# Kernel tuning notes

Hardware: AMD Instinct MI355X
Metric: run time of the kernel (lower is better)

## Reference

```python
import jax, jax.numpy as jnp
import numpy as np

N, E, D, H = 50000, 800000, 128, 128


def setup_inputs() -> dict:
    key = jax.random.key(0)
    ks = jax.random.split(key, 8)
    x = jax.random.normal(ks[0], (N, D), dtype=jnp.float32)
    src = jax.random.randint(ks[1], (E,), 0, N, dtype=jnp.int64)
    dst = jax.random.randint(ks[2], (E,), 0, N, dtype=jnp.int64)
    s_in = 1.0 / np.sqrt(D)
    s_h = 1.0 / np.sqrt(H)
    return {
        "x": x,
        "src": src,
        "dst": dst,
        "W_self1": jax.random.normal(ks[3], (D, H), dtype=jnp.float32) * s_in,
        "W_neigh1": jax.random.normal(ks[4], (D, H), dtype=jnp.float32) * s_in,
        "b1": jnp.zeros((H,), dtype=jnp.float32),
        "W_self2": jax.random.normal(ks[5], (H, H), dtype=jnp.float32) * s_h,
        "W_neigh2": jax.random.normal(ks[6], (H, H), dtype=jnp.float32) * s_h,
        "b2": jnp.zeros((H,), dtype=jnp.float32),
    }


def _sage_conv(h, src, dst, n_nodes, W_self, W_neigh, b):
    # mean aggregation over in-neighbors: gather src feats, segment-sum by dst
    msg = jax.ops.segment_sum(h[src], dst, num_segments=n_nodes)  # [N, d]
    deg = jax.ops.segment_sum(jnp.ones((src.shape[0], 1), h.dtype), dst,
                              num_segments=n_nodes)               # [N, 1]
    h_neigh = msg / jnp.maximum(deg, 1.0)  # zero-degree nodes -> 0 (DGL clamps)
    return h @ W_self + h_neigh @ W_neigh + b


def reference(x, src, dst, W_self1, W_neigh1, b1, W_self2, W_neigh2, b2):
    n = x.shape[0]
    h = jax.nn.relu(_sage_conv(x, src, dst, n, W_self1, W_neigh1, b1))
    return _sage_conv(h, src, dst, n, W_self2, W_neigh2, b2)
```

## Files before the change

### kernel.cpp

```cpp
#include <hip/hip_runtime.h>

#define DH 128
#define SLOTS 64

typedef __bf16 bf16x8 __attribute__((ext_vector_type(8)));
typedef float f32x4 __attribute__((ext_vector_type(4)));
typedef float f32x2 __attribute__((ext_vector_type(2)));

__device__ __forceinline__ ushort f2b(float f) {
  union { float f; unsigned u; } c; c.f = f;
  unsigned u = c.u;
  unsigned r = (u + 0x7fffu + ((u >> 16) & 1u)) >> 16;
  return (ushort)r;
}
__device__ __forceinline__ unsigned char f2f8(float v) {
  return (unsigned char)(__builtin_amdgcn_cvt_pk_fp8_f32(v, v, 0, false) & 0xff);
}

__global__ void k_prep(int4* __restrict__ degz, int nZero, int nz4,
                       const float* __restrict__ x, ushort* __restrict__ xb,
                       uint2* __restrict__ xf8, long n8, int nConv,
                       const float* __restrict__ Ws1, const float* __restrict__ Wn1,
                       const float* __restrict__ Ws2, const float* __restrict__ Wn2,
                       ushort* __restrict__ Wp1, ushort* __restrict__ Wp2) {
  int bid = blockIdx.x;
  if (bid < nZero) {
    int i = bid * 256 + threadIdx.x;
    if (i < nz4) degz[i] = int4{0, 0, 0, 0};
  } else if (bid < nZero + nConv) {
    long i = (long)(bid - nZero) * 256 + threadIdx.x;
    if (i >= n8) return;
    const float4* p = (const float4*)x + i * 2;
    float4 a = p[0], b = p[1];
    uint4 o;
    o.x = (unsigned)f2b(a.x) | ((unsigned)f2b(a.y) << 16);
    o.y = (unsigned)f2b(a.z) | ((unsigned)f2b(a.w) << 16);
    o.z = (unsigned)f2b(b.x) | ((unsigned)f2b(b.y) << 16);
    o.w = (unsigned)f2b(b.z) | ((unsigned)f2b(b.w) << 16);
    ((uint4*)xb)[i] = o;
    int w0 = __builtin_amdgcn_cvt_pk_fp8_f32(a.x, a.y, 0, false);
    w0 = __builtin_amdgcn_cvt_pk_fp8_f32(a.z, a.w, w0, true);
    int w1 = __builtin_amdgcn_cvt_pk_fp8_f32(b.x, b.y, 0, false);
    w1 = __builtin_amdgcn_cvt_pk_fp8_f32(b.z, b.w, w1, true);
    xf8[i] = uint2{(unsigned)w0, (unsigned)w1};
  } else {
    int idx = (bid - nZero - nConv) * 256 + threadIdx.x;
    if (idx >= 2 * 8 * 8 * 64 * 8) return;
    int layer = idx >> 15;
    int t = idx & 32767;
    int j = t & 7;
    int lane = (t >> 3) & 63;
    int cb = (t >> 9) & 7;
    int s = (t >> 12) & 7;
    int col = cb * 16 + (lane & 15);
    int k = s * 32 + ((lane >> 4) * 8) + j;
    const float* Wself = layer ? Ws2 : Ws1;
    const float* Wneigh = layer ? Wn2 : Wn1;
    float v = (k < 128) ? Wself[k * 128 + col] : Wneigh[(k - 128) * 128 + col];
    (layer ? Wp2 : Wp1)[t] = f2b(v);
  }
}

__global__ void k_fill8p(const int* __restrict__ src, const int* __restrict__ dst,
                         int* __restrict__ deg, int* __restrict__ colsrc,
                         int E, int nper, int chunkSz) {
  int part = blockIdx.x & 7;
  int chunk = blockIdx.x >> 3;
  int lo = part * nper, hi = lo + nper;
  int base = chunk * chunkSz;
  int end = min(base + chunkSz, E);
  for (int i = base + threadIdx.x; i < end; i += 256) {
    int d = dst[i];
    int s = src[i];
    if (d >= lo && d < hi) {
      int r = atomicAdd(&deg[d], 1);
      if (r < SLOTS) colsrc[(size_t)d * SLOTS + r] = s;
    }
  }
}

__device__ __forceinline__ void acc8f8(float* a, uint2 v) {
  f32x2 p0 = __builtin_amdgcn_cvt_pk_f32_fp8(v.x, false);
  f32x2 p1 = __builtin_amdgcn_cvt_pk_f32_fp8(v.x, true);
  f32x2 p2 = __builtin_amdgcn_cvt_pk_f32_fp8(v.y, false);
  f32x2 p3 = __builtin_amdgcn_cvt_pk_f32_fp8(v.y, true);
  a[0] += p0.x; a[1] += p0.y; a[2] += p1.x; a[3] += p1.y;
  a[4] += p2.x; a[5] += p2.y; a[6] += p3.x; a[7] += p3.y;
}

template <int RELU, int OUTF32, int WRITEF8>
__global__ __launch_bounds__(1024, 8) void k_aggemm(
    const ushort* __restrict__ feat, const uint2* __restrict__ feat8,
    const int* __restrict__ deg, const int* __restrict__ colsrc,
    const ushort* __restrict__ Wp, const float* __restrict__ bias,
    void* __restrict__ outp, unsigned char* __restrict__ outf8, int M) {
  __shared__ ushort hn[64][136];
  int tid = threadIdx.x;

  {
    int g = tid >> 4, l = tid & 15;
    int node = blockIdx.x * 64 + g;
    float a[8] = {0.f, 0.f, 0.f, 0.f, 0.f, 0.f, 0.f, 0.f};
    float sc = 0.f;
    if (node < M) {
      int dd = min(deg[node], SLOTS);
      const int* cs = colsrc + (size_t)node * SLOTS;
      int e = 0;
      for (; e + 8 <= dd; e += 8) {
        int s0 = cs[e], s1 = cs[e + 1], s2 = cs[e + 2], s3 = cs[e + 3];
        int s4 = cs[e + 4], s5 = cs[e + 5], s6 = cs[e + 6], s7 = cs[e + 7];
        uint2 v0 = feat8[(size_t)s0 * 16 + l];
        uint2 v1 = feat8[(size_t)s1 * 16 + l];
        uint2 v2 = feat8[(size_t)s2 * 16 + l];
        uint2 v3 = feat8[(size_t)s3 * 16 + l];
        uint2 v4 = feat8[(size_t)s4 * 16 + l];
        uint2 v5 = feat8[(size_t)s5 * 16 + l];
        uint2 v6 = feat8[(size_t)s6 * 16 + l];
        uint2 v7 = feat8[(size_t)s7 * 16 + l];
        acc8f8(a, v0); acc8f8(a, v1); acc8f8(a, v2); acc8f8(a, v3);
        acc8f8(a, v4); acc8f8(a, v5); acc8f8(a, v6); acc8f8(a, v7);
      }
      for (; e + 4 <= dd; e += 4) {
        int s0 = cs[e], s1 = cs[e + 1], s2 = cs[e + 2], s3 = cs[e + 3];
        uint2 v0 = feat8[(size_t)s0 * 16 + l];
        uint2 v1 = feat8[(size_t)s1 * 16 + l];
        uint2 v2 = feat8[(size_t)s2 * 16 + l];
        uint2 v3 = feat8[(size_t)s3 * 16 + l];
        acc8f8(a, v0); acc8f8(a, v1); acc8f8(a, v2); acc8f8(a, v3);
      }
      for (; e < dd; ++e) acc8f8(a, feat8[(size_t)cs[e] * 16 + l]);
      sc = 1.0f / fmaxf((float)dd, 1.0f);
    }
    uint4 o;
    o.x = (unsigned)f2b(a[0] * sc) | ((unsigned)f2b(a[1] * sc) << 16);
    o.y = (unsigned)f2b(a[2] * sc) | ((unsigned)f2b(a[3] * sc) << 16);
    o.z = (unsigned)f2b(a[4] * sc) | ((unsigned)f2b(a[5] * sc) << 16);
    o.w = (unsigned)f2b(a[6] * sc) | ((unsigned)f2b(a[7] * sc) << 16);
    *(uint4*)&hn[g][l * 8] = o;
  }
  __syncthreads();

  int wave = tid >> 6, lane = tid & 63;
  int rg = wave >> 2;
  int cb0 = (wave & 3) * 2;
  int rowA = blockIdx.x * 64 + rg * 16 + (lane & 15);
  int kq = lane >> 4;
  bool valid = rowA < M;
  size_t abase = (size_t)rowA * DH + kq * 8;
  int lrow = rg * 16 + (lane & 15);
  f32x4 acc0 = {}, acc1 = {};
#pragma unroll
  for (int hf = 0; hf < 2; ++hf) {
#pragma unroll
    for (int ks = 0; ks < 4; ++ks) {
      bf16x8 a = {};
      if (hf == 0) {
        if (valid) a = __builtin_bit_cast(bf16x8, *(const uint4*)(feat + abase + ks * 32));
      } else {
        a = __builtin_bit_cast(bf16x8, *(const uint4*)&hn[lrow][ks * 32 + kq * 8]);
      }
      int sg = hf * 4 + ks;
      const ushort* wp = Wp + sg * 4096 + lane * 8;
      bf16x8 b0 = __builtin_bit_cast(bf16x8, *(const uint4*)(wp + cb0 * 512));
      bf16x8 b1 = __builtin_bit_cast(bf16x8, *(const uint4*)(wp + (cb0 + 1) * 512));
      acc0 = __builtin_amdgcn_mfma_f32_16x16x32_bf16(a, b0, acc0, 0, 0, 0);
      acc1 = __builtin_amdgcn_mfma_f32_16x16x32_bf16(a, b1, acc1, 0, 0, 0);
    }
  }
  int col = lane & 15;
  int row0 = blockIdx.x * 64 + rg * 16 + (lane >> 4) * 4;
#pragma unroll
  for (int t = 0; t < 2; ++t) {
    int cb = cb0 + t;
    float bv = bias[cb * 16 + col];
    f32x4 acc = t ? acc1 : acc0;
#pragma unroll
    for (int j = 0; j < 4; ++j) {
      int rr = row0 + j;
      if (rr < M) {
        float v = acc[j] + bv;
        if (RELU) v = fmaxf(v, 0.f);
        if (OUTF32)
          ((float*)outp)[(size_t)rr * DH + cb * 16 + col] = v;
        else
          ((ushort*)outp)[(size_t)rr * DH + cb * 16 + col] = f2b(v);
        if (WRITEF8)
          outf8[(size_t)rr * DH + cb * 16 + col] = f2f8(v);
      }
    }
  }
}

extern "C" void kernel_launch(void* const* d_in, const int* in_sizes, int n_in,
                              void* d_out, int out_size, void* d_ws, size_t ws_size,
                              hipStream_t stream) {
  const float* x = (const float*)d_in[0];
  const int* src = (const int*)d_in[1];
  const int* dst = (const int*)d_in[2];
  const float* Wself1 = (const float*)d_in[3];
  const float* Wneigh1 = (const float*)d_in[4];
  const float* b1 = (const float*)d_in[5];
  const float* Wself2 = (const float*)d_in[6];
  const float* Wneigh2 = (const float*)d_in[7];
  const float* b2 = (const float*)d_in[8];
  int N = in_sizes[0] / DH;
  int E = in_sizes[1];

  char* w = (char*)d_ws;
  auto alloc = [&](size_t bytes) {
    char* p = w;
    w += (bytes + 255) & ~(size_t)255;
    return p;
  };
  ushort* xb = (ushort*)alloc((size_t)N * DH * 2);
  ushort* hb = (ushort*)alloc((size_t)N * DH * 2);
  unsigned char* xf8 = (unsigned char*)alloc((size_t)N * DH);
  unsigned char* hf8 = (unsigned char*)alloc((size_t)N * DH);
  ushort* Wp1 = (ushort*)alloc(32768 * 2);
  ushort* Wp2 = (ushort*)alloc(32768 * 2);
  int* deg = (int*)alloc((size_t)N * 4);
  int* colsrc = (int*)alloc((size_t)N * SLOTS * 4);

  int nz4 = (N + 3) / 4;
  int nZero = (nz4 + 255) / 256;
  long n8 = (long)N * DH / 8;
  int nConv = (int)((n8 + 255) / 256);
  int nPack = (2 * 8 * 8 * 64 * 8 + 255) / 256;
  k_prep<<<nZero + nConv + nPack, 256, 0, stream>>>(
      (int4*)deg, nZero, nz4, x, xb, (uint2*)xf8, n8, nConv,
      Wself1, Wneigh1, Wself2, Wneigh2, Wp1, Wp2);

  int nper = (N + 7) / 8;
  int nchunk = 256;
  int chunkSz = (E + nchunk - 1) / nchunk;
  k_fill8p<<<nchunk * 8, 256, 0, stream>>>(src, dst, deg, colsrc, E, nper, chunkSz);

  int gb = (N + 63) / 64;
  k_aggemm<1, 0, 1><<<gb, 1024, 0, stream>>>(xb, (const uint2*)xf8, deg, colsrc,
                                             Wp1, b1, hb, hf8, N);
  k_aggemm<0, 1, 0><<<gb, 1024, 0, stream>>>(hb, (const uint2*)hf8, deg, colsrc,
                                             Wp2, b2, d_out, nullptr, N);
}
```

Before: 129.1 us.

## Pre-bucket edges by destination range before CSR slot fill

```diff
diff --git a/kernel.cpp b/kernel.cpp
--- a/kernel.cpp
+++ b/kernel.cpp
@@ -2,6 +2,7 @@
 
 #define DH 128
 #define SLOTS 64
+#define BSH 13
 
 typedef __bf16 bf16x8 __attribute__((ext_vector_type(8)));
 typedef float f32x4 __attribute__((ext_vector_type(4)));
@@ -61,21 +62,54 @@
   }
 }
 
-__global__ void k_fill8p(const int* __restrict__ src, const int* __restrict__ dst,
-                         int* __restrict__ deg, int* __restrict__ colsrc,
-                         int E, int nper, int chunkSz) {
-  int part = blockIdx.x & 7;
+__global__ void k_bucket(const int* __restrict__ src, const int* __restrict__ dst,
+                         uint2* __restrict__ ebuf, int* __restrict__ gcnt,
+                         int E, int cap) {
+  __shared__ int cnt[8], base[8], cur[8];
+  int csz = (E + gridDim.x - 1) / gridDim.x;
+  int beg = blockIdx.x * csz;
+  int end = min(beg + csz, E);
+  for (int r = beg; r < end; r += 256) {
+    int i = r + threadIdx.x;
+    int b = 0, d = 0, s = 0;
+    if (threadIdx.x < 8) cnt[threadIdx.x] = 0;
+    __syncthreads();
+    bool live = i < end;
+    if (live) {
+      d = dst[i];
+      s = src[i];
+      b = d >> BSH;
+      atomicAdd(&cnt[b], 1);
+    }
+    __syncthreads();
+    if (threadIdx.x < 8) {
+      base[threadIdx.x] = cnt[threadIdx.x] ? atomicAdd(&gcnt[threadIdx.x], cnt[threadIdx.x]) : 0;
+      cur[threadIdx.x] = 0;
+    }
+    __syncthreads();
+    if (live) {
+      int rk = atomicAdd(&cur[b], 1);
+      int pos = base[b] + rk;
+      if (pos < cap) ebuf[(size_t)b * cap + pos] = uint2{(unsigned)s, (unsigned)d};
+    }
+    __syncthreads();
+  }
+}
+
+__global__ void k_fillB(const uint2* __restrict__ ebuf, const int* __restrict__ gcnt,
+                        int* __restrict__ deg, int* __restrict__ colsrc, int cap) {
+  int p = blockIdx.x & 7;
   int chunk = blockIdx.x >> 3;
-  int lo = part * nper, hi = lo + nper;
-  int base = chunk * chunkSz;
-  int end = min(base + chunkSz, E);
-  for (int i = base + threadIdx.x; i < end; i += 256) {
-    int d = dst[i];
-    int s = src[i];
-    if (d >= lo && d < hi) {
-      int r = atomicAdd(&deg[d], 1);
-      if (r < SLOTS) colsrc[(size_t)d * SLOTS + r] = s;
-    }
+  int cnt = min(gcnt[p], cap);
+  int len = (cnt + 127) >> 7;
+  int beg = chunk * len;
+  int end = min(beg + len, cnt);
+  const uint2* eb = ebuf + (size_t)p * cap;
+  for (int i = beg + threadIdx.x; i < end; i += 256) {
+    uint2 e = eb[i];
+    int d = (int)e.y;
+    int r = atomicAdd(&deg[d], 1);
+    if (r < SLOTS) colsrc[(size_t)d * SLOTS + r] = (int)e.x;
   }
 }
 
@@ -218,10 +252,13 @@
   unsigned char* hf8 = (unsigned char*)alloc((size_t)N * DH);
   ushort* Wp1 = (ushort*)alloc(32768 * 2);
   ushort* Wp2 = (ushort*)alloc(32768 * 2);
-  int* deg = (int*)alloc((size_t)N * 4);
+  int* deg = (int*)alloc(((size_t)N + 8) * 4);
+  int* gcnt = deg + N;
   int* colsrc = (int*)alloc((size_t)N * SLOTS * 4);
-
-  int nz4 = (N + 3) / 4;
+  int cap = E / 8 + 65536;
+  uint2* ebuf = (uint2*)alloc((size_t)8 * cap * 8);
+
+  int nz4 = (N + 8 + 3) / 4;
   int nZero = (nz4 + 255) / 256;
   long n8 = (long)N * DH / 8;
   int nConv = (int)((n8 + 255) / 256);
@@ -230,10 +267,8 @@
       (int4*)deg, nZero, nz4, x, xb, (uint2*)xf8, n8, nConv,
       Wself1, Wneigh1, Wself2, Wneigh2, Wp1, Wp2);
 
-  int nper = (N + 7) / 8;
-  int nchunk = 256;
-  int chunkSz = (E + nchunk - 1) / nchunk;
-  k_fill8p<<<nchunk * 8, 256, 0, stream>>>(src, dst, deg, colsrc, E, nper, chunkSz);
+  k_bucket<<<256, 256, 0, stream>>>(src, dst, ebuf, gcnt, E, cap);
+  k_fillB<<<128 * 8, 256, 0, stream>>>(ebuf, gcnt, deg, colsrc, cap);
 
   int gb = (N + 63) / 64;
   k_aggemm<1, 0, 1><<<gb, 1024, 0, stream>>>(xb, (const uint2*)xf8, deg, colsrc,
```

New measurement: 166.4 us. 28.9% more time.
